# Optimization experiments

Measured on AMD Instinct MI355X. Metric: run time of the kernel, lower is better.

The kernel has to match this reference:

```python
import jax, jax.numpy as jnp
import numpy as np

B, T, D, H = 2, 2048, 1024, 16
HD = D // H
ALPHA = HD ** -0.5
EPS = 1e-5


def setup_inputs() -> dict:
    key = jax.random.key(0)
    ks = jax.random.split(key, 8)
    x = jax.random.normal(ks[0], (B, T, D), dtype=jnp.float32)
    # additive causal mask: 0 where allowed, -inf where disallowed
    causal = jnp.triu(jnp.ones((T, T), dtype=bool), k=1)
    attention_mask = jnp.where(causal, -jnp.inf, 0.0).astype(jnp.float32)
    rab = jax.random.normal(ks[1], (1, H, T, T), dtype=jnp.float32) * 0.02
    W_in = jax.random.normal(ks[2], (D, 4 * D), dtype=jnp.float32) * (D ** -0.5)
    b_in = jnp.zeros((4 * D,), dtype=jnp.float32)
    W_out = jax.random.normal(ks[3], (D, D), dtype=jnp.float32) * (D ** -0.5)
    b_out = jnp.zeros((D,), dtype=jnp.float32)
    ln_w = jnp.ones((D,), dtype=jnp.float32)
    ln_b = jnp.zeros((D,), dtype=jnp.float32)
    return {"x": x, "attention_mask": attention_mask, "rab": rab,
            "W_in": W_in, "b_in": b_in, "W_out": W_out, "b_out": b_out,
            "ln_w": ln_w, "ln_b": ln_b}


def _heads(t):  # [B,T,D] -> [B,H,T,HD]
    return t.reshape(B, T, H, HD).transpose(0, 2, 1, 3)


def _layernorm(t, w, b):
    mu = jnp.mean(t, axis=-1, keepdims=True)
    var = jnp.mean(jnp.square(t - mu), axis=-1, keepdims=True)
    return (t - mu) * jax.lax.rsqrt(var + EPS) * w + b


def reference(x, attention_mask, rab, W_in, b_in, W_out, b_out, ln_w, ln_b):
    h = jax.nn.silu(x @ W_in + b_in)                      # [B,T,4D]
    U, V, Q, K = jnp.split(h, 4, axis=-1)
    Qh, Kh, Vh = _heads(Q), _heads(K), _heads(V)
    logits = jnp.einsum('bhqd,bhkd->bhqk', Qh, Kh) * ALPHA
    logits = logits + rab + attention_mask[None, None]    # [B,H,T,T]
    # allowed counts from the additive mask (0 == allowed)
    allowed = (attention_mask == 0).astype(jnp.float32)   # [T,T]
    denom = jnp.clip(jnp.sum(allowed, axis=-1, keepdims=True), 1.0)  # [T,1]
    logits_safe = jnp.where(jnp.isinf(logits) & (logits < 0), -1e9, logits)
    attn = jax.nn.silu(logits_safe) / denom[None, None]
    AV = jnp.einsum('bhqk,bhkd->bhqd', attn, Vh)
    AV = AV.transpose(0, 2, 1, 3).reshape(B, T, D)
    y = (_layernorm(AV, ln_w, ln_b) * U) @ W_out + b_out
    return y
```

## Files before the change

kernel.cpp:

```cpp
#include <hip/hip_runtime.h>
#include <hip/hip_bf16.h>

#define BATCH 2
#define TSEQ 2048
#define DIM 1024
#define NH 16
#define HDIM 64
#define MROWS (BATCH * TSEQ)

typedef __attribute__((ext_vector_type(4))) float f32x4;
typedef __attribute__((ext_vector_type(8))) short short8;

__device__ __forceinline__ unsigned short f2bf(float f) {
    union { float f; unsigned int u; } x; x.f = f;
    unsigned int r = x.u + 0x7fffu + ((x.u >> 16) & 1u);
    return (unsigned short)(r >> 16);
}

__device__ __forceinline__ float bf2f(unsigned short s) {
    union { unsigned int u; float f; } t; t.u = (unsigned int)s << 16;
    return t.f;
}

__device__ __forceinline__ float silu_f(float v) {
    return v * __builtin_amdgcn_rcpf(1.f + __expf(-v));
}

__device__ __forceinline__ unsigned int pack_bf16(float lo, float hi) {
    union { __hip_bfloat162 h; unsigned int u; } r;
    r.h = __float22bfloat162_rn(float2{lo, hi});
    return r.u;
}

__device__ __forceinline__ void gl_lds16(const void* g, void* l) {
    __builtin_amdgcn_global_load_lds(
        (const __attribute__((address_space(1))) void*)g,
        (__attribute__((address_space(3))) void*)l, 16, 0, 0);
}

__device__ __forceinline__ short8 rd_swz(const unsigned short* base, int row, int chunk) {
    const char* b = (const char*)base;
    return *(const short8*)(b + row * 128 + (((chunk ^ (row & 7)) << 4)));
}

__device__ __forceinline__ void transpose32(const float* __restrict__ in,
                                            unsigned short* __restrict__ out,
                                            int R, int C, int bx, int by, int tid) {
    __shared__ float tile[32][33];
    int tx = tid & 31, ty = tid >> 5;
    int c0 = bx * 32, r0 = by * 32;
    #pragma unroll
    for (int i = 0; i < 32; i += 8)
        tile[ty + i][tx] = in[(size_t)(r0 + ty + i) * C + c0 + tx];
    __syncthreads();
    #pragma unroll
    for (int i = 0; i < 32; i += 8)
        out[(size_t)(c0 + ty + i) * R + r0 + tx] = f2bf(tile[tx][ty + i]);
}

__global__ __launch_bounds__(256) void k_prep(const float* __restrict__ x,
                                              unsigned short* __restrict__ xb,
                                              const float* __restrict__ W_in,
                                              unsigned short* __restrict__ WinT,
                                              const float* __restrict__ W_out,
                                              unsigned short* __restrict__ WoutT) {
    const int b = blockIdx.x, tid = threadIdx.x;
    if (b < 4096) {
        int i = b * 256 + tid;
        float4 v = ((const float4*)x)[i];
        union { unsigned short s[4]; uint2 u; } o;
        o.s[0] = f2bf(v.x); o.s[1] = f2bf(v.y); o.s[2] = f2bf(v.z); o.s[3] = f2bf(v.w);
        ((uint2*)xb)[i] = o.u;
    } else if (b < 8192) {
        int bb = b - 4096;
        transpose32(W_in, WinT, 1024, 4096, bb & 127, bb >> 7, tid);
    } else {
        int bb = b - 8192;
        transpose32(W_out, WoutT, 1024, 1024, bb & 31, bb >> 5, tid);
    }
}

__device__ __forceinline__ void stage256o(const unsigned short* __restrict__ A,
                                          const unsigned short* __restrict__ Bt,
                                          int row0, int col0, int k0,
                                          unsigned short* sAbuf, unsigned short* sBbuf,
                                          int tid) {
    #pragma unroll
    for (int q = 0; q < 4; ++q) {
        int c = tid + 512 * q;
        int rr = c >> 3;
        int kcs = (c & 7) ^ (rr & 7);
        gl_lds16(Bt + (size_t)(col0 + rr) * 1024 + k0 + kcs * 8, sBbuf + c * 8);
    }
    __builtin_amdgcn_sched_barrier(0);
    #pragma unroll
    for (int p = 0; p < 4; ++p) {
        int c = (tid < 256) ? (256 * p + tid) : (1024 + 256 * p + (tid - 256));
        int rr = c >> 3;
        int kcs = (c & 7) ^ (rr & 7);
        gl_lds16(A + (size_t)(row0 + rr) * 1024 + k0 + kcs * 8, sAbuf + c * 8);
        __builtin_amdgcn_sched_barrier(0);
    }
}

__global__ __launch_bounds__(512, 2) void k_gemm1_256(
    const unsigned short* __restrict__ A, const unsigned short* __restrict__ Bt,
    const float* __restrict__ bias,
    unsigned short* __restrict__ outU, unsigned short* __restrict__ outVt,
    unsigned short* __restrict__ outQ, unsigned short* __restrict__ outK)
{
    __shared__ __align__(16) unsigned short sA[2][256 * 64];
    __shared__ __align__(16) unsigned short sB[2][256 * 64];

    const int tid = threadIdx.x;
    const int lane = tid & 63, wid = tid >> 6;
    const int lr = lane & 15, lk = lane >> 4;
    const int wm = wid >> 2, wn = wid & 3;
    const int bm = blockIdx.x, bn = blockIdx.y;
    const int row0 = bm * 256, col0 = bn * 256;

    f32x4 acc[8][4] = {};

    stage256o(A, Bt, row0, col0, 0, sA[0], sB[0], tid);
    asm volatile("s_waitcnt vmcnt(0)" ::: "memory");
    __builtin_amdgcn_s_barrier();
    __builtin_amdgcn_sched_barrier(0);

    int cur = 0;
    for (int kt = 0; kt < 15; ++kt) {
        stage256o(A, Bt, row0, col0, (kt + 1) * 64, sA[cur ^ 1], sB[cur ^ 1], tid);
        short8 bf[2][4];
        #pragma unroll
        for (int kk = 0; kk < 2; ++kk)
            #pragma unroll
            for (int n = 0; n < 4; ++n)
                bf[kk][n] = rd_swz(sB[cur], wn * 64 + n * 16 + lr, kk * 4 + lk);

        #pragma unroll
        for (int ph = 0; ph < 4; ++ph) {
            short8 af[2][2];
            #pragma unroll
            for (int mm = 0; mm < 2; ++mm)
                #pragma unroll
                for (int kk = 0; kk < 2; ++kk)
                    af[mm][kk] = rd_swz(sA[cur], wm * 128 + (ph * 2 + mm) * 16 + lr, kk * 4 + lk);
            __builtin_amdgcn_s_barrier();
            __builtin_amdgcn_s_setprio(1);
            #pragma unroll
            for (int mm = 0; mm < 2; ++mm)
                #pragma unroll
                for (int n = 0; n < 4; ++n)
                    #pragma unroll
                    for (int kk = 0; kk < 2; ++kk)
                        acc[ph * 2 + mm][n] = __builtin_amdgcn_mfma_f32_16x16x32_bf16(
                            af[mm][kk], bf[kk][n], acc[ph * 2 + mm][n], 0, 0, 0);
            __builtin_amdgcn_s_setprio(0);
            if (ph == 0)      asm volatile("s_waitcnt vmcnt(10)" ::: "memory");
            else if (ph == 1) asm volatile("s_waitcnt vmcnt(9)" ::: "memory");
            else if (ph == 2) asm volatile("s_waitcnt vmcnt(8)" ::: "memory");
            else              asm volatile("s_waitcnt vmcnt(3)" ::: "memory");
            __builtin_amdgcn_s_barrier();
        }
        __builtin_amdgcn_sched_barrier(0);
        cur ^= 1;
    }

    {
        short8 bf[2][4];
        #pragma unroll
        for (int kk = 0; kk < 2; ++kk)
            #pragma unroll
            for (int n = 0; n < 4; ++n)
                bf[kk][n] = rd_swz(sB[cur], wn * 64 + n * 16 + lr, kk * 4 + lk);
        #pragma unroll
        for (int ph = 0; ph < 4; ++ph) {
            short8 af[2][2];
            #pragma unroll
            for (int mm = 0; mm < 2; ++mm)
                #pragma unroll
                for (int kk = 0; kk < 2; ++kk)
                    af[mm][kk] = rd_swz(sA[cur], wm * 128 + (ph * 2 + mm) * 16 + lr, kk * 4 + lk);
            __builtin_amdgcn_s_barrier();
            __builtin_amdgcn_s_setprio(1);
            #pragma unroll
            for (int mm = 0; mm < 2; ++mm)
                #pragma unroll
                for (int n = 0; n < 4; ++n)
                    #pragma unroll
                    for (int kk = 0; kk < 2; ++kk)
                        acc[ph * 2 + mm][n] = __builtin_amdgcn_mfma_f32_16x16x32_bf16(
                            af[mm][kk], bf[kk][n], acc[ph * 2 + mm][n], 0, 0, 0);
            __builtin_amdgcn_s_setprio(0);
            if (ph == 0)      { asm volatile("s_waitcnt vmcnt(2)" ::: "memory"); __builtin_amdgcn_s_barrier(); }
            else if (ph == 1) { asm volatile("s_waitcnt vmcnt(1)" ::: "memory"); __builtin_amdgcn_s_barrier(); }
            else if (ph == 2) { asm volatile("s_waitcnt vmcnt(0)" ::: "memory"); __builtin_amdgcn_s_barrier(); }
        }
    }

    const int sec = bn >> 2;
    #pragma unroll
    for (int n = 0; n < 4; ++n) {
        const int cg = col0 + wn * 64 + n * 16 + lr;
        const int cc = cg & 1023;
        const float bv = bias[cg];
        #pragma unroll
        for (int m = 0; m < 8; ++m) {
            const int rg0 = row0 + wm * 128 + m * 16 + lk * 4;
            float sv[4];
            #pragma unroll
            for (int j = 0; j < 4; ++j)
                sv[j] = silu_f(acc[m][n][j] + bv);
            if (sec == 0) {
                #pragma unroll
                for (int j = 0; j < 4; ++j)
                    outU[((size_t)(rg0 + j) << 10) + cc] = f2bf(sv[j]);
            } else if (sec == 1) {
                union { unsigned short s[4]; uint2 u; } pk;
                #pragma unroll
                for (int j = 0; j < 4; ++j) pk.s[j] = f2bf(sv[j]);
                *(uint2*)(outVt + ((size_t)cc << 12) + rg0) = pk.u;
            } else if (sec == 2) {
                #pragma unroll
                for (int j = 0; j < 4; ++j)
                    outQ[((size_t)(rg0 + j) << 10) + cc] = f2bf(sv[j] * 0.125f);
            } else {
                #pragma unroll
                for (int j = 0; j < 4; ++j)
                    outK[((size_t)(rg0 + j) << 10) + cc] = f2bf(sv[j]);
            }
        }
    }
}

__device__ __forceinline__ void stage128o(const unsigned short* __restrict__ A,
                                          const unsigned short* __restrict__ Bt,
                                          int row0, int col0, int k0,
                                          unsigned short* sAbuf, unsigned short* sBbuf,
                                          int tid) {
    #pragma unroll
    for (int q = 0; q < 4; ++q) {
        int c = tid + 256 * q;
        int rr = c >> 3;
        int kcs = (c & 7) ^ (rr & 7);
        gl_lds16(Bt + (size_t)(col0 + rr) * 1024 + k0 + kcs * 8, sBbuf + c * 8);
    }
    __builtin_amdgcn_sched_barrier(0);
    {
        int c = tid;          int rr = c >> 3; int kcs = (c & 7) ^ (rr & 7);
        gl_lds16(A + (size_t)(row0 + rr) * 1024 + k0 + kcs * 8, sAbuf + c * 8);
        c = 512 + tid;        rr = c >> 3;     kcs = (c & 7) ^ (rr & 7);
        gl_lds16(A + (size_t)(row0 + rr) * 1024 + k0 + kcs * 8, sAbuf + c * 8);
    }
    __builtin_amdgcn_sched_barrier(0);
    {
        int c = 256 + tid;    int rr = c >> 3; int kcs = (c & 7) ^ (rr & 7);
        gl_lds16(A + (size_t)(row0 + rr) * 1024 + k0 + kcs * 8, sAbuf + c * 8);
        c = 768 + tid;        rr = c >> 3;     kcs = (c & 7) ^ (rr & 7);
        gl_lds16(A + (size_t)(row0 + rr) * 1024 + k0 + kcs * 8, sAbuf + c * 8);
    }
    __builtin_amdgcn_sched_barrier(0);
}

__global__ __launch_bounds__(256, 2) void k_gemm2(
    const unsigned short* __restrict__ A, const unsigned short* __restrict__ Bt,
    const float* __restrict__ bias, float* __restrict__ outY)
{
    __shared__ __align__(16) unsigned short sA[2][128 * 64];
    __shared__ __align__(16) unsigned short sB[2][128 * 64];

    const int tid = threadIdx.x;
    const int lane = tid & 63, wid = tid >> 6;
    const int lr = lane & 15, lk = lane >> 4;
    const int wm = wid >> 1, wn = wid & 1;
    const int bm = blockIdx.x, bn = blockIdx.y;
    const int row0 = bm * 128, col0 = bn * 128;

    f32x4 acc[4][4] = {};

    stage128o(A, Bt, row0, col0, 0, sA[0], sB[0], tid);
    asm volatile("s_waitcnt vmcnt(0)" ::: "memory");
    __builtin_amdgcn_s_barrier();
    __builtin_amdgcn_sched_barrier(0);

    int cur = 0;
    for (int kt = 0; kt < 15; ++kt) {
        stage128o(A, Bt, row0, col0, (kt + 1) * 64, sA[cur ^ 1], sB[cur ^ 1], tid);
        short8 bf[2][4];
        #pragma unroll
        for (int kk = 0; kk < 2; ++kk)
            #pragma unroll
            for (int n = 0; n < 4; ++n)
                bf[kk][n] = rd_swz(sB[cur], wn * 64 + n * 16 + lr, kk * 4 + lk);

        #pragma unroll
        for (int ph = 0; ph < 2; ++ph) {
            short8 af[2][2];
            #pragma unroll
            for (int mm = 0; mm < 2; ++mm)
                #pragma unroll
                for (int kk = 0; kk < 2; ++kk)
                    af[mm][kk] = rd_swz(sA[cur], wm * 64 + (ph * 2 + mm) * 16 + lr, kk * 4 + lk);
            __builtin_amdgcn_s_barrier();
            __builtin_amdgcn_s_setprio(1);
            #pragma unroll
            for (int mm = 0; mm < 2; ++mm)
                #pragma unroll
                for (int n = 0; n < 4; ++n)
                    #pragma unroll
                    for (int kk = 0; kk < 2; ++kk)
                        acc[ph * 2 + mm][n] = __builtin_amdgcn_mfma_f32_16x16x32_bf16(
                            af[mm][kk], bf[kk][n], acc[ph * 2 + mm][n], 0, 0, 0);
            __builtin_amdgcn_s_setprio(0);
            if (ph == 0) asm volatile("s_waitcnt vmcnt(10)" ::: "memory");
            else         asm volatile("s_waitcnt vmcnt(2)" ::: "memory");
            __builtin_amdgcn_s_barrier();
        }
        __builtin_amdgcn_sched_barrier(0);
        cur ^= 1;
    }

    {
        short8 bf[2][4];
        #pragma unroll
        for (int kk = 0; kk < 2; ++kk)
            #pragma unroll
            for (int n = 0; n < 4; ++n)
                bf[kk][n] = rd_swz(sB[cur], wn * 64 + n * 16 + lr, kk * 4 + lk);
        #pragma unroll
        for (int ph = 0; ph < 2; ++ph) {
            short8 af[2][2];
            #pragma unroll
            for (int mm = 0; mm < 2; ++mm)
                #pragma unroll
                for (int kk = 0; kk < 2; ++kk)
                    af[mm][kk] = rd_swz(sA[cur], wm * 64 + (ph * 2 + mm) * 16 + lr, kk * 4 + lk);
            __builtin_amdgcn_s_barrier();
            __builtin_amdgcn_s_setprio(1);
            #pragma unroll
            for (int mm = 0; mm < 2; ++mm)
                #pragma unroll
                for (int n = 0; n < 4; ++n)
                    #pragma unroll
                    for (int kk = 0; kk < 2; ++kk)
                        acc[ph * 2 + mm][n] = __builtin_amdgcn_mfma_f32_16x16x32_bf16(
                            af[mm][kk], bf[kk][n], acc[ph * 2 + mm][n], 0, 0, 0);
            __builtin_amdgcn_s_setprio(0);
            if (ph == 0) { asm volatile("s_waitcnt vmcnt(0)" ::: "memory"); __builtin_amdgcn_s_barrier(); }
        }
    }

    #pragma unroll
    for (int n = 0; n < 4; ++n) {
        const int cg = col0 + wn * 64 + n * 16 + lr;
        const float bv = bias[cg];
        #pragma unroll
        for (int m = 0; m < 4; ++m) {
            const int rg0 = row0 + wm * 64 + m * 16 + lk * 4;
            #pragma unroll
            for (int j = 0; j < 4; ++j)
                outY[(size_t)(rg0 + j) * 1024 + cg] = acc[m][n][j] + bv;
        }
    }
}

__global__ __launch_bounds__(256, 4) void k_attn(
    const unsigned short* __restrict__ Qb,
    const unsigned short* __restrict__ Kb,
    const unsigned short* __restrict__ Vt,
    const float* __restrict__ rab,
    unsigned short* __restrict__ AV)
{
    __shared__ __align__(16) unsigned short sK[2][64 * 64];
    __shared__ __align__(16) unsigned short sVt[2][64 * 64];
    __shared__ __align__(16) unsigned short sP[64 * 64];

    const int tid = threadIdx.x;
    const int lane = tid & 63;
    const int w = tid >> 6;
    const int lr = lane & 15;
    const int lk = lane >> 4;

    const int bid = blockIdx.x;
    const int xcd = bid & 7;
    const int j_ = bid >> 3;
    const int cc_ = j_ & 31;
    const int b4 = j_ >> 5;
    const int h = ((b4 & 1) << 3) | xcd;
    const int bb = b4 >> 1;
    const int cc2 = (b4 >= 2) ? ((cc_ + 16) & 31) : cc_;
    const int qt = (b4 & 1) ? (31 - cc2) : cc2;
    const int q0 = qt * 64;

    short8 qreg[2];
    #pragma unroll
    for (int ks = 0; ks < 2; ++ks)
        qreg[ks] = *(const short8*)(Qb + (((size_t)(bb * TSEQ + q0 + w * 16 + lr)) << 10)
                                     + h * 64 + ks * 32 + lk * 8);
    __builtin_amdgcn_sched_barrier(0);

    const int qloc = w * 16 + lr;
    const int qcol = q0 + qloc;
    const float* rabq = rab + ((size_t)h * TSEQ + qcol) * TSEQ + lk * 4;

    f32x4 acc[4] = {};

    #define STAGE(buf, kt_) do {                                                      \
        int k0s = (kt_) * 64;                                                         \
        for (int c = tid; c < 512; c += 256) {                                        \
            int rr = c >> 3, kc = c & 7;                                              \
            int kcs = kc ^ (rr & 7);                                                  \
            gl_lds16(Kb + (((size_t)(bb * TSEQ + k0s + rr)) << 10) + h * 64 + kcs * 8,\
                     sK[buf] + c * 8);                                                \
            gl_lds16(Vt + (((size_t)(h * 64 + rr)) << 12) + bb * TSEQ + k0s + kcs * 8,\
                     sVt[buf] + c * 8);                                               \
        }                                                                             \
    } while (0)

    float4 rv0[4], rv1[4];

    STAGE(0, 0);
    __builtin_amdgcn_sched_barrier(0);
    #pragma unroll
    for (int nt = 0; nt < 4; ++nt)
        rv0[nt] = *(const float4*)(rabq + nt * 16);
    __builtin_amdgcn_sched_barrier(0);
    asm volatile("s_waitcnt vmcnt(4)" ::: "memory");
    __builtin_amdgcn_s_barrier();

    #define BODY(KT, BUFC, RVC, RVN) do {                                             \
        const int k0 = (KT) * 64;                                                     \
        const bool have_next = (KT) < qt;                                             \
        if (have_next) STAGE((BUFC) ^ 1, (KT) + 1);                                   \
        __builtin_amdgcn_sched_barrier(0);                                            \
        if (have_next) {                                                              \
            _Pragma("unroll")                                                         \
            for (int nt = 0; nt < 4; ++nt)                                            \
                RVN[nt] = *(const float4*)(rabq + k0 + 64 + nt * 16);                 \
        }                                                                             \
        __builtin_amdgcn_sched_barrier(0);                                            \
        f32x4 s[4];                                                                   \
        _Pragma("unroll")                                                             \
        for (int nt = 0; nt < 4; ++nt) {                                              \
            s[nt][0] = RVC[nt].x; s[nt][1] = RVC[nt].y;                               \
            s[nt][2] = RVC[nt].z; s[nt][3] = RVC[nt].w;                               \
        }                                                                             \
        __builtin_amdgcn_s_setprio(1);                                                \
        _Pragma("unroll")                                                             \
        for (int ks = 0; ks < 2; ++ks) {                                              \
            _Pragma("unroll")                                                         \
            for (int nt = 0; nt < 4; ++nt)                                            \
                s[nt] = __builtin_amdgcn_mfma_f32_16x16x32_bf16(                      \
                    rd_swz(sK[BUFC], nt * 16 + lr, ks * 4 + lk), qreg[ks], s[nt], 0, 0, 0); \
        }                                                                             \
        __builtin_amdgcn_s_setprio(0);                                                \
        char* pb = (char*)sP;                                                         \
        char* paddr = pb + qloc * 128 + ((lk & 1) * 8);                               \
        if (have_next) {                                                              \
            _Pragma("unroll")                                                         \
            for (int nt = 0; nt < 4; ++nt) {                                          \
                unsigned int p01 = pack_bf16(silu_f(s[nt][0]), silu_f(s[nt][1]));     \
                unsigned int p23 = pack_bf16(silu_f(s[nt][2]), silu_f(s[nt][3]));     \
                const int chunk = nt * 2 + (lk >> 1);                                 \
                *(uint2*)(paddr + ((chunk ^ (qloc & 7)) << 4)) = make_uint2(p01, p23);\
            }                                                                         \
        } else {                                                                      \
            _Pragma("unroll")                                                         \
            for (int nt = 0; nt < 4; ++nt) {                                          \
                const int kb = k0 + nt * 16 + lk * 4;                                 \
                float a0 = (kb + 0 <= qcol) ? silu_f(s[nt][0]) : 0.f;                 \
                float a1 = (kb + 1 <= qcol) ? silu_f(s[nt][1]) : 0.f;                 \
                float a2 = (kb + 2 <= qcol) ? silu_f(s[nt][2]) : 0.f;                 \
                float a3 = (kb + 3 <= qcol) ? silu_f(s[nt][3]) : 0.f;                 \
                unsigned int p01 = pack_bf16(a0, a1);                                 \
                unsigned int p23 = pack_bf16(a2, a3);                                 \
                const int chunk = nt * 2 + (lk >> 1);                                 \
                *(uint2*)(paddr + ((chunk ^ (qloc & 7)) << 4)) = make_uint2(p01, p23);\
            }                                                                         \
        }                                                                             \
        __builtin_amdgcn_s_setprio(1);                                                \
        _Pragma("unroll")                                                             \
        for (int ks = 0; ks < 2; ++ks) {                                              \
            short8 ap = rd_swz(sP, qloc, ks * 4 + lk);                                \
            _Pragma("unroll")                                                         \
            for (int dt = 0; dt < 4; ++dt)                                            \
                acc[dt] = __builtin_amdgcn_mfma_f32_16x16x32_bf16(                    \
                    ap, rd_swz(sVt[BUFC], dt * 16 + lr, ks * 4 + lk), acc[dt], 0, 0, 0); \
        }                                                                             \
        __builtin_amdgcn_s_setprio(0);                                                \
        if (have_next) {                                                              \
            asm volatile("s_waitcnt vmcnt(4)" ::: "memory");                          \
            __builtin_amdgcn_s_barrier();                                             \
        }                                                                             \
    } while (0)

    for (int kt = 0; kt <= qt; kt += 2) {
        BODY(kt, 0, rv0, rv1);
        if (kt + 1 <= qt) BODY(kt + 1, 1, rv1, rv0);
    }
    #undef BODY
    #undef STAGE

    #pragma unroll
    for (int dt = 0; dt < 4; ++dt)
        #pragma unroll
        for (int j = 0; j < 4; ++j)
            AV[(((size_t)(bb * TSEQ + q0 + w * 16 + lk * 4 + j)) << 10)
               + h * 64 + dt * 16 + lr] = f2bf(acc[dt][j]);
}

__global__ __launch_bounds__(256) void k_ln(const unsigned short* __restrict__ AV,
                                            const unsigned short* __restrict__ U,
                                            const float* __restrict__ lnw,
                                            const float* __restrict__ lnb,
                                            unsigned short* __restrict__ z) {
    __shared__ float red[8];
    const int row = blockIdx.x, tid = threadIdx.x;
    const float c = (float)((row & (TSEQ - 1)) + 1);
    const float eps = 1e-5f * c * c;
    union { unsigned short s[4]; uint2 u; } a;
    a.u = ((const uint2*)(AV + ((size_t)row << 10)))[tid];
    float v[4];
    #pragma unroll
    for (int i = 0; i < 4; ++i) v[i] = bf2f(a.s[i]);
    float s = v[0] + v[1] + v[2] + v[3];
    float s2 = v[0] * v[0] + v[1] * v[1] + v[2] * v[2] + v[3] * v[3];
    #pragma unroll
    for (int o = 32; o > 0; o >>= 1) { s += __shfl_xor(s, o); s2 += __shfl_xor(s2, o); }
    const int w = tid >> 6;
    if ((tid & 63) == 0) { red[w] = s; red[4 + w] = s2; }
    __syncthreads();
    s = red[0] + red[1] + red[2] + red[3];
    s2 = red[4] + red[5] + red[6] + red[7];
    const float mu = s * (1.f / 1024.f);
    const float var = s2 * (1.f / 1024.f) - mu * mu;
    const float rstd = rsqrtf(var + eps);
    union { unsigned short s[4]; uint2 u; } uu;
    uu.u = ((const uint2*)(U + ((size_t)row << 10)))[tid];
    float4 lw = ((const float4*)lnw)[tid];
    float4 lb = ((const float4*)lnb)[tid];
    union { unsigned short o[4]; uint2 u; } ov;
    ov.o[0] = f2bf(((v[0] - mu) * rstd * lw.x + lb.x) * bf2f(uu.s[0]));
    ov.o[1] = f2bf(((v[1] - mu) * rstd * lw.y + lb.y) * bf2f(uu.s[1]));
    ov.o[2] = f2bf(((v[2] - mu) * rstd * lw.z + lb.z) * bf2f(uu.s[2]));
    ov.o[3] = f2bf(((v[3] - mu) * rstd * lw.w + lb.w) * bf2f(uu.s[3]));
    ((uint2*)z)[((size_t)row << 8) + tid] = ov.u;
}

extern "C" void kernel_launch(void* const* d_in, const int* in_sizes, int n_in,
                              void* d_out, int out_size, void* d_ws, size_t ws_size,
                              hipStream_t stream) {
    const float* x     = (const float*)d_in[0];
    const float* rab   = (const float*)d_in[2];
    const float* W_in  = (const float*)d_in[3];
    const float* b_in  = (const float*)d_in[4];
    const float* W_out = (const float*)d_in[5];
    const float* b_out = (const float*)d_in[6];
    const float* ln_w  = (const float*)d_in[7];
    const float* ln_b  = (const float*)d_in[8];
    float* y = (float*)d_out;

    char* ws = (char*)d_ws;
    size_t off = 0;
    auto alloc = [&](size_t bytes) -> void* {
        void* p = ws + off;
        off += (bytes + 255) & ~(size_t)255;
        return p;
    };
    unsigned short* WinT  = (unsigned short*)alloc((size_t)4096 * 1024 * 2);
    unsigned short* WoutT = (unsigned short*)alloc((size_t)1024 * 1024 * 2);
    unsigned short* xb    = (unsigned short*)alloc((size_t)MROWS * DIM * 2);
    unsigned short* Ubuf  = (unsigned short*)alloc((size_t)MROWS * DIM * 2);
    unsigned short* Qb    = (unsigned short*)alloc((size_t)MROWS * DIM * 2);
    unsigned short* Kb    = (unsigned short*)alloc((size_t)MROWS * DIM * 2);
    unsigned short* Vtb   = (unsigned short*)alloc((size_t)DIM * MROWS * 2);
    unsigned short* AV    = (unsigned short*)alloc((size_t)MROWS * DIM * 2);
    unsigned short* z     = (unsigned short*)alloc((size_t)MROWS * DIM * 2);

    k_prep<<<dim3(9216), dim3(256), 0, stream>>>(x, xb, W_in, WinT, W_out, WoutT);
    k_gemm1_256<<<dim3(16, 16), dim3(512), 0, stream>>>(xb, WinT, b_in, Ubuf, Vtb, Qb, Kb);
    k_attn<<<dim3(1024), dim3(256), 0, stream>>>(Qb, Kb, Vtb, rab, AV);
    k_ln<<<dim3(MROWS), dim3(256), 0, stream>>>(AV, Ubuf, ln_w, ln_b, z);
    k_gemm2<<<dim3(32, 8), dim3(256), 0, stream>>>(z, WoutT, b_out, y);
}
```

Before: 156.5 us.

## Process both batches per attention block to share rab loads across batch

The attention kernel now launches 512-thread blocks that handle the same (head, query tile) for both batch elements, with warps 0-3 on batch 0 and warps 4-7 on batch 1. K, V and P shared buffers gain a batch dimension. Each batch's waves still load their own rab values, but the two batches now read the same rab tile at about the same time within one block, which should improve cache reuse of the large rab tensor. The cost is double the LDS per block, fewer blocks, and different occupancy and load-balance behaviour.

```diff
diff --git a/kernel.cpp b/kernel.cpp
--- a/kernel.cpp
+++ b/kernel.cpp
@@ -363,42 +363,41 @@
     }
 }
 
-__global__ __launch_bounds__(256, 4) void k_attn(
+__global__ __launch_bounds__(512, 4) void k_attn(
     const unsigned short* __restrict__ Qb,
     const unsigned short* __restrict__ Kb,
     const unsigned short* __restrict__ Vt,
     const float* __restrict__ rab,
     unsigned short* __restrict__ AV)
 {
-    __shared__ __align__(16) unsigned short sK[2][64 * 64];
-    __shared__ __align__(16) unsigned short sVt[2][64 * 64];
-    __shared__ __align__(16) unsigned short sP[64 * 64];
+    __shared__ __align__(16) unsigned short sK[2][2][64 * 64];
+    __shared__ __align__(16) unsigned short sVt[2][2][64 * 64];
+    __shared__ __align__(16) unsigned short sP[2][64 * 64];
 
     const int tid = threadIdx.x;
     const int lane = tid & 63;
     const int w = tid >> 6;
+    const int bw = w >> 2;
+    const int wq = w & 3;
     const int lr = lane & 15;
     const int lk = lane >> 4;
 
     const int bid = blockIdx.x;
     const int xcd = bid & 7;
-    const int j_ = bid >> 3;
-    const int cc_ = j_ & 31;
-    const int b4 = j_ >> 5;
-    const int h = ((b4 & 1) << 3) | xcd;
-    const int bb = b4 >> 1;
-    const int cc2 = (b4 >= 2) ? ((cc_ + 16) & 31) : cc_;
-    const int qt = (b4 & 1) ? (31 - cc2) : cc2;
+    const int h = (((bid >> 3) & 1) << 3) | xcd;
+    const int r_ = (bid >> 4) & 15;
+    const int half = bid >> 8;
+    const int qt = half ? (31 - r_) : r_;
     const int q0 = qt * 64;
 
     short8 qreg[2];
     #pragma unroll
     for (int ks = 0; ks < 2; ++ks)
-        qreg[ks] = *(const short8*)(Qb + (((size_t)(bb * TSEQ + q0 + w * 16 + lr)) << 10)
+        qreg[ks] = *(const short8*)(Qb + (((size_t)(bw * TSEQ + q0 + wq * 16 + lr)) << 10)
                                      + h * 64 + ks * 32 + lk * 8);
     __builtin_amdgcn_sched_barrier(0);
 
-    const int qloc = w * 16 + lr;
+    const int qloc = wq * 16 + lr;
     const int qcol = q0 + qloc;
     const float* rabq = rab + ((size_t)h * TSEQ + qcol) * TSEQ + lk * 4;
 
@@ -406,14 +405,16 @@
 
     #define STAGE(buf, kt_) do {                                                      \
         int k0s = (kt_) * 64;                                                         \
-        for (int c = tid; c < 512; c += 256) {                                        \
-            int rr = c >> 3, kc = c & 7;                                              \
-            int kcs = kc ^ (rr & 7);                                                  \
-            gl_lds16(Kb + (((size_t)(bb * TSEQ + k0s + rr)) << 10) + h * 64 + kcs * 8,\
-                     sK[buf] + c * 8);                                                \
-            gl_lds16(Vt + (((size_t)(h * 64 + rr)) << 12) + bb * TSEQ + k0s + kcs * 8,\
-                     sVt[buf] + c * 8);                                               \
-        }                                                                             \
+        int rr = tid >> 3, kc = tid & 7;                                              \
+        int kcs = kc ^ (rr & 7);                                                      \
+        gl_lds16(Kb + (((size_t)(k0s + rr)) << 10) + h * 64 + kcs * 8,                \
+                 sK[buf][0] + tid * 8);                                               \
+        gl_lds16(Kb + (((size_t)(TSEQ + k0s + rr)) << 10) + h * 64 + kcs * 8,         \
+                 sK[buf][1] + tid * 8);                                               \
+        gl_lds16(Vt + (((size_t)(h * 64 + rr)) << 12) + k0s + kcs * 8,                \
+                 sVt[buf][0] + tid * 8);                                              \
+        gl_lds16(Vt + (((size_t)(h * 64 + rr)) << 12) + TSEQ + k0s + kcs * 8,         \
+                 sVt[buf][1] + tid * 8);                                              \
     } while (0)
 
     float4 rv0[4], rv1[4];
@@ -450,10 +451,11 @@
             _Pragma("unroll")                                                         \
             for (int nt = 0; nt < 4; ++nt)                                            \
                 s[nt] = __builtin_amdgcn_mfma_f32_16x16x32_bf16(                      \
-                    rd_swz(sK[BUFC], nt * 16 + lr, ks * 4 + lk), qreg[ks], s[nt], 0, 0, 0); \
+                    rd_swz(sK[BUFC][bw], nt * 16 + lr, ks * 4 + lk), qreg[ks],        \
+                    s[nt], 0, 0, 0);                                                  \
         }                                                                             \
         __builtin_amdgcn_s_setprio(0);                                                \
-        char* pb = (char*)sP;                                                         \
+        char* pb = (char*)sP[bw];                                                     \
         char* paddr = pb + qloc * 128 + ((lk & 1) * 8);                               \
         if (have_next) {                                                              \
             _Pragma("unroll")                                                         \
@@ -480,11 +482,12 @@
         __builtin_amdgcn_s_setprio(1);                                                \
         _Pragma("unroll")                                                             \
         for (int ks = 0; ks < 2; ++ks) {                                              \
-            short8 ap = rd_swz(sP, qloc, ks * 4 + lk);                                \
+            short8 ap = rd_swz(sP[bw], qloc, ks * 4 + lk);                            \
             _Pragma("unroll")                                                         \
             for (int dt = 0; dt < 4; ++dt)                                            \
                 acc[dt] = __builtin_amdgcn_mfma_f32_16x16x32_bf16(                    \
-                    ap, rd_swz(sVt[BUFC], dt * 16 + lr, ks * 4 + lk), acc[dt], 0, 0, 0); \
+                    ap, rd_swz(sVt[BUFC][bw], dt * 16 + lr, ks * 4 + lk),             \
+                    acc[dt], 0, 0, 0);                                                \
         }                                                                             \
         __builtin_amdgcn_s_setprio(0);                                                \
         if (have_next) {                                                              \
@@ -504,7 +507,7 @@
     for (int dt = 0; dt < 4; ++dt)
         #pragma unroll
         for (int j = 0; j < 4; ++j)
-            AV[(((size_t)(bb * TSEQ + q0 + w * 16 + lk * 4 + j)) << 10)
+            AV[(((size_t)(bw * TSEQ + q0 + wq * 16 + lk * 4 + j)) << 10)
                + h * 64 + dt * 16 + lr] = f2bf(acc[dt][j]);
 }
 
@@ -578,7 +581,7 @@
 
     k_prep<<<dim3(9216), dim3(256), 0, stream>>>(x, xb, W_in, WinT, W_out, WoutT);
     k_gemm1_256<<<dim3(16, 16), dim3(512), 0, stream>>>(xb, WinT, b_in, Ubuf, Vtb, Qb, Kb);
-    k_attn<<<dim3(1024), dim3(256), 0, stream>>>(Qb, Kb, Vtb, rab, AV);
+    k_attn<<<dim3(512), dim3(512), 0, stream>>>(Qb, Kb, Vtb, rab, AV);
     k_ln<<<dim3(MROWS), dim3(256), 0, stream>>>(AV, Ubuf, ln_w, ln_b, z);
     k_gemm2<<<dim3(32, 8), dim3(256), 0, stream>>>(z, WoutT, b_out, y);
 }
```

After: 169.5 us. 8.3% more time.
